# Optimization experiments

Measured on AMD Instinct MI355X. Metric: run time of the kernel, lower is better.

## Reference

```python
import jax, jax.numpy as jnp
import numpy as np
from jax import lax


def _prelu(x, a):
    return jnp.where(x >= 0, x, a * x)


def setup_inputs() -> dict:
    key = jax.random.key(0)
    ks = jax.random.split(key, 6)
    T, B, I, H = 2048, 64, 256, 256
    return {
        "sequences": jax.random.normal(ks[0], (T, B, I), dtype=jnp.float32),
        "W_f": jax.random.normal(ks[1], (I, H), dtype=jnp.float32) * (2.0 / (I + H)) ** 0.5,
        "U_f": jax.random.normal(ks[2], (H, H), dtype=jnp.float32) * (1.0 / H) ** 0.5,
        "b_f": jnp.ones((H,), dtype=jnp.float32),  # chrono-init bias ~ log(U(1,T_max))
        "W_h": jax.random.normal(ks[3], (I, H), dtype=jnp.float32) * (2.0 / (I + H)) ** 0.5,
        "U_h": jax.random.normal(ks[4], (H, H), dtype=jnp.float32) * (1.0 / H) ** 0.5,
        "b_h": jnp.zeros((H,), dtype=jnp.float32),
        "prelu_a": jnp.full((1,), 0.25, dtype=jnp.float32),
    }


def reference(sequences, W_f, U_f, b_f, W_h, U_h, b_h, prelu_a):
    # sequences: [T, B, I] time-major. Precompute input projections once
    # (hoists the big GEMMs out of the sequential recurrence).
    xf = jnp.einsum('tbi,ih->tbh', sequences, W_f) + b_f  # [T,B,H]
    xh = jnp.einsum('tbi,ih->tbh', sequences, W_h) + b_h  # [T,B,H]

    # First step: last_h is None -> no U terms, no f*last_h term.
    f0 = jax.nn.sigmoid(xf[0])
    h0 = _prelu((1.0 - f0) * jnp.tanh(xh[0]), prelu_a)  # [B,H]

    def step(h, xs):
        xf_t, xh_t = xs
        f = jax.nn.sigmoid(h @ U_f + xf_t)
        h_new = f * h + (1.0 - f) * jnp.tanh(h @ U_h + xh_t)
        h_new = _prelu(h_new, prelu_a)
        return h_new, h_new

    _, hs = lax.scan(step, h0, (xf[1:], xh[1:]))  # [T-1,B,H]
    all_h = jnp.concatenate([h0[None], hs], axis=0)  # [T,B,H]
    # torch.cat(hs) concatenates along dim 0 -> [T*B, H]
    return all_h.reshape(-1, all_h.shape[-1])
```

## Files before the change

kernel.cpp:

```cpp
#include <hip/hip_runtime.h>


#define T_STEPS 2048
#define BATCH   64
#define NCOL    512

typedef _Float16 half_t;
typedef half_t half2_t __attribute__((ext_vector_type(2)));
typedef half_t half4_t __attribute__((ext_vector_type(4)));

__device__ __forceinline__ float4 ld4(const float* p) { return *(const float4*)p; }
__device__ __forceinline__ void fma4(float4& acc, float s, const float4& v) {
  acc.x = fmaf(s, v.x, acc.x); acc.y = fmaf(s, v.y, acc.y);
  acc.z = fmaf(s, v.z, acc.z); acc.w = fmaf(s, v.w, acc.w);
}

__device__ __forceinline__ void store_xt(float* p, const float4& v) { *(float4*)p = v; }
__device__ __forceinline__ void store_xt(half_t* p, const float4& v) {
  half4_t h;
  h.x = (half_t)v.x; h.y = (half_t)v.y; h.z = (half_t)v.z; h.w = (half_t)v.w;
  *(half4_t*)p = h;
}
__device__ __forceinline__ float xload(const float* p) { return *p; }
__device__ __forceinline__ float xload(const half_t* p) { return (float)*p; }

#if __has_builtin(__builtin_amdgcn_fdot2)
__device__ __forceinline__ float fdot2(half2_t a, half2_t b, float c) {
  return __builtin_amdgcn_fdot2(a, b, c, false);
}
#else
__device__ __forceinline__ float fdot2(half2_t a, half2_t b, float c) {
  return c + (float)a.x * (float)b.x + (float)a.y * (float)b.y;
}
#endif

__device__ __forceinline__ half2_t bcast_h2(float f) {
  return __builtin_bit_cast(half2_t, f);
}

template <typename XT>
__global__ __launch_bounds__(256, 4)
void xproj_gemm(const float* __restrict__ seq,
                const float* __restrict__ Wf, const float* __restrict__ bf,
                const float* __restrict__ Wh, const float* __restrict__ bh,
                XT* __restrict__ xfh)
{
  __shared__ float As[32 * 132];
  __shared__ float Bs[32 * 132];
  const int tid = threadIdx.x;
  const int mt = blockIdx.x >> 2;
  const int nt = blockIdx.x & 3;
  const int m0 = mt * 128;
  const int n0 = nt * 128;
  const int tm = tid >> 4;
  const int tn = tid & 15;

  float4 acc[8][2];
  #pragma unroll
  for (int i = 0; i < 8; ++i) {
    acc[i][0] = make_float4(0.f, 0.f, 0.f, 0.f);
    acc[i][1] = make_float4(0.f, 0.f, 0.f, 0.f);
  }

  const float* bsrc  = (n0 < 256) ? Wf : Wh;
  const int    bcol0 = (n0 < 256) ? n0 : (n0 - 256);

  for (int kt = 0; kt < 8; ++kt) {
    const int k0 = kt * 32;
    #pragma unroll
    for (int p = 0; p < 4; ++p) {
      int idx = p * 256 + tid;
      int r   = idx >> 3;
      int c4  = idx & 7;
      float4 v = ld4(seq + (size_t)(m0 + r) * 256 + k0 + c4 * 4);
      As[(c4*4+0)*132 + r] = v.x;
      As[(c4*4+1)*132 + r] = v.y;
      As[(c4*4+2)*132 + r] = v.z;
      As[(c4*4+3)*132 + r] = v.w;
    }
    #pragma unroll
    for (int p = 0; p < 4; ++p) {
      int idx = p * 256 + tid;
      int kr  = idx >> 5;
      int c4  = idx & 31;
      float4 v = ld4(bsrc + (size_t)(k0 + kr) * 256 + bcol0 + c4 * 4);
      *(float4*)&Bs[kr*132 + c4*4] = v;
    }
    __syncthreads();
    #pragma unroll
    for (int k = 0; k < 32; ++k) {
      float4 a0 = ld4(&As[k*132 + tm*4]);
      float4 a1 = ld4(&As[k*132 + 64 + tm*4]);
      float4 b0 = ld4(&Bs[k*132 + tn*4]);
      float4 b1 = ld4(&Bs[k*132 + 64 + tn*4]);
      float ar[8] = {a0.x, a0.y, a0.z, a0.w, a1.x, a1.y, a1.z, a1.w};
      #pragma unroll
      for (int i = 0; i < 8; ++i) {
        fma4(acc[i][0], ar[i], b0);
        fma4(acc[i][1], ar[i], b1);
      }
    }
    __syncthreads();
  }

  const float* bias_src = (n0 < 256) ? bf : bh;
  float4 bias0 = ld4(bias_src + bcol0 + tn*4);
  float4 bias1 = ld4(bias_src + bcol0 + 64 + tn*4);
  #pragma unroll
  for (int i = 0; i < 8; ++i) {
    int m = m0 + ((i < 4) ? (tm*4 + i) : (64 + tm*4 + (i - 4)));
    float4 r0 = acc[i][0];
    r0.x += bias0.x; r0.y += bias0.y; r0.z += bias0.z; r0.w += bias0.w;
    float4 r1 = acc[i][1];
    r1.x += bias1.x; r1.y += bias1.y; r1.z += bias1.z; r1.w += bias1.w;
    store_xt(xfh + (size_t)m * NCOL + n0 + tn*4,      r0);
    store_xt(xfh + (size_t)m * NCOL + n0 + 64 + tn*4, r1);
  }
}

template <typename XT>
__global__ __launch_bounds__(512, 2)
void janet_rec(const float* __restrict__ Uf, const float* __restrict__ Uh,
               const XT* __restrict__ xfh, const float* __restrict__ pa,
               float* __restrict__ out)
{
  __shared__ __align__(16) half_t h_lds[256];
  __shared__ float g_lds[256];
  const int tid = threadIdx.x;
  const int b   = blockIdx.x;
  const int kg  = tid & 7;
  const int jg  = tid >> 3;
  const int j0  = jg * 8;

  const float* Usrc = (j0 < 256) ? (Uf + j0) : (Uh + (j0 - 256));
  half2_t u2[8][16];
  #pragma unroll
  for (int p = 0; p < 16; ++p) {
    const int k = kg * 32 + 2 * p;
    #pragma unroll
    for (int j = 0; j < 8; ++j) {
      half2_t w;
      w.x = (half_t)Usrc[(size_t)k * 256 + j];
      w.y = (half_t)Usrc[(size_t)(k + 1) * 256 + j];
      u2[j][p] = w;
    }
  }

  const float aprelu = pa[0];
  if (tid < 256) h_lds[tid] = (half_t)0.f;
  float h_old = 0.f;
  __syncthreads();

  float x = xload(xfh + (size_t)b * NCOL + tid);

  for (int t = 0; t < T_STEPS; ++t) {
    float x_next = 0.f;
    if (t + 1 < T_STEPS)
      x_next = xload(xfh + ((size_t)(t + 1) * BATCH + b) * NCOL + tid);

    const float4* hv4 = (const float4*)(h_lds + kg * 32);
    float4 ha = hv4[0], hb = hv4[1], hc = hv4[2], hd = hv4[3];
    half2_t hp[16];
    hp[0]  = bcast_h2(ha.x); hp[1]  = bcast_h2(ha.y);
    hp[2]  = bcast_h2(ha.z); hp[3]  = bcast_h2(ha.w);
    hp[4]  = bcast_h2(hb.x); hp[5]  = bcast_h2(hb.y);
    hp[6]  = bcast_h2(hb.z); hp[7]  = bcast_h2(hb.w);
    hp[8]  = bcast_h2(hc.x); hp[9]  = bcast_h2(hc.y);
    hp[10] = bcast_h2(hc.z); hp[11] = bcast_h2(hc.w);
    hp[12] = bcast_h2(hd.x); hp[13] = bcast_h2(hd.y);
    hp[14] = bcast_h2(hd.z); hp[15] = bcast_h2(hd.w);

    float acc[8];
    #pragma unroll
    for (int j = 0; j < 8; ++j) acc[j] = 0.f;
    #pragma unroll
    for (int p = 0; p < 16; ++p) {
      const half2_t hv = hp[p];
      #pragma unroll
      for (int j = 0; j < 8; ++j)
        acc[j] = fdot2(hv, u2[j][p], acc[j]);
    }

    float s00 = acc[0] + __shfl_xor(acc[0], 1);
    float s01 = acc[1] + __shfl_xor(acc[1], 1);
    float s02 = acc[2] + __shfl_xor(acc[2], 1);
    float s03 = acc[3] + __shfl_xor(acc[3], 1);
    float s04 = acc[4] + __shfl_xor(acc[4], 1);
    float s05 = acc[5] + __shfl_xor(acc[5], 1);
    float s06 = acc[6] + __shfl_xor(acc[6], 1);
    float s07 = acc[7] + __shfl_xor(acc[7], 1);
    const bool sb0 = (kg & 1);
    float r0 = sb0 ? s01 : s00;
    float r1 = sb0 ? s03 : s02;
    float r2 = sb0 ? s05 : s04;
    float r3 = sb0 ? s07 : s06;
    r0 += __shfl_xor(r0, 2);
    r1 += __shfl_xor(r1, 2);
    r2 += __shfl_xor(r2, 2);
    r3 += __shfl_xor(r3, 2);
    const bool sb1 = (kg & 2);
    float q0 = sb1 ? r1 : r0;
    float q1 = sb1 ? r3 : r2;
    q0 += __shfl_xor(q0, 4);
    q1 += __shfl_xor(q1, 4);
    const float s = (kg & 4) ? q1 : q0;

    const float pre = s + x;
    float f = 0.f;
    if (tid < 256) {
      f = __builtin_amdgcn_rcpf(1.f + __expf(-pre));
    } else {
      float e2 = __expf(2.f * pre);
      float g  = 1.f - 2.f * __builtin_amdgcn_rcpf(e2 + 1.f);
      g_lds[tid - 256] = g;
    }
    __syncthreads();
    if (tid < 256) {
      float g  = g_lds[tid];
      float hn = fmaf(f, h_old - g, g);
      hn = (hn >= 0.f) ? hn : aprelu * hn;
      h_old = hn;
      h_lds[tid] = (half_t)hn;
      out[((size_t)t * BATCH + b) * 256 + tid] = hn;
    }
    __syncthreads();
    x = x_next;
  }
}

extern "C" void kernel_launch(void* const* d_in, const int* in_sizes, int n_in,
                              void* d_out, int out_size, void* d_ws, size_t ws_size,
                              hipStream_t stream) {
  const float* seq = (const float*)d_in[0];
  const float* Wf  = (const float*)d_in[1];
  const float* Uf  = (const float*)d_in[2];
  const float* bf  = (const float*)d_in[3];
  const float* Wh  = (const float*)d_in[4];
  const float* Uh  = (const float*)d_in[5];
  const float* bh  = (const float*)d_in[6];
  const float* pa  = (const float*)d_in[7];
  float* out = (float*)d_out;

  const size_t rows = (size_t)T_STEPS * BATCH;
  const size_t need_f32 = rows * NCOL * sizeof(float);

  dim3 g1(4096), blk1(256);
  dim3 g2(BATCH), blk2(512);

  if (ws_size >= need_f32) {
    float* xfh = (float*)d_ws;
    hipLaunchKernelGGL(xproj_gemm<float>, g1, blk1, 0, stream, seq, Wf, bf, Wh, bh, xfh);
    hipLaunchKernelGGL(janet_rec<float>,  g2, blk2, 0, stream, Uf, Uh, xfh, pa, out);
  } else {
    half_t* xfh = (half_t*)d_ws;
    hipLaunchKernelGGL(xproj_gemm<half_t>, g1, blk1, 0, stream, seq, Wf, bf, Wh, bh, xfh);
    hipLaunchKernelGGL(janet_rec<half_t>,  g2, blk2, 0, stream, Uf, Uh, xfh, pa, out);
  }
}
```

Measured before the change: 2.533 ms.

## Use MFMA for the recurrent matmul with 16 batch rows per block

Replaces the per-batch fdot2 recurrence with MFMA 16x16x32 f16 instructions. Each block now handles 16 batch rows, and each wave computes a 32-column slice of both the f and h gates, so the gate math fuses with no cross-thread g exchange. Hidden state is double-buffered in swizzled LDS, which needs only one barrier per step. The grid shrinks from 64 blocks to 4, so far fewer CUs are used, and the per-step x loads are no longer prefetched.

```diff
diff --git a/kernel.cpp b/kernel.cpp
--- a/kernel.cpp
+++ b/kernel.cpp
@@ -4,10 +4,12 @@
 #define T_STEPS 2048
 #define BATCH   64
 #define NCOL    512
+#define MB      16
 
 typedef _Float16 half_t;
-typedef half_t half2_t __attribute__((ext_vector_type(2)));
+typedef half_t f16x8  __attribute__((ext_vector_type(8)));
 typedef half_t half4_t __attribute__((ext_vector_type(4)));
+typedef float  f32x4  __attribute__((ext_vector_type(4)));
 
 __device__ __forceinline__ float4 ld4(const float* p) { return *(const float4*)p; }
 __device__ __forceinline__ void fma4(float4& acc, float s, const float4& v) {
@@ -23,20 +25,6 @@
 }
 __device__ __forceinline__ float xload(const float* p) { return *p; }
 __device__ __forceinline__ float xload(const half_t* p) { return (float)*p; }
-
-#if __has_builtin(__builtin_amdgcn_fdot2)
-__device__ __forceinline__ float fdot2(half2_t a, half2_t b, float c) {
-  return __builtin_amdgcn_fdot2(a, b, c, false);
-}
-#else
-__device__ __forceinline__ float fdot2(half2_t a, half2_t b, float c) {
-  return c + (float)a.x * (float)b.x + (float)a.y * (float)b.y;
-}
-#endif
-
-__device__ __forceinline__ half2_t bcast_h2(float f) {
-  return __builtin_bit_cast(half2_t, f);
-}
 
 template <typename XT>
 __global__ __launch_bounds__(256, 4)
@@ -124,107 +112,113 @@
                const XT* __restrict__ xfh, const float* __restrict__ pa,
                float* __restrict__ out)
 {
-  __shared__ __align__(16) half_t h_lds[256];
-  __shared__ float g_lds[256];
-  const int tid = threadIdx.x;
-  const int b   = blockIdx.x;
-  const int kg  = tid & 7;
-  const int jg  = tid >> 3;
-  const int j0  = jg * 8;
-
-  const float* Usrc = (j0 < 256) ? (Uf + j0) : (Uh + (j0 - 256));
-  half2_t u2[8][16];
-  #pragma unroll
-  for (int p = 0; p < 16; ++p) {
-    const int k = kg * 32 + 2 * p;
-    #pragma unroll
-    for (int j = 0; j < 8; ++j) {
-      half2_t w;
-      w.x = (half_t)Usrc[(size_t)k * 256 + j];
-      w.y = (half_t)Usrc[(size_t)(k + 1) * 256 + j];
-      u2[j][p] = w;
+  __shared__ __align__(16) half_t hbuf[2][MB * 256];
+  const int tid  = threadIdx.x;
+  const int wave = tid >> 6;
+  const int lane = tid & 63;
+  const int l15  = lane & 15;
+  const int lk   = lane >> 4;
+  const int wcol = wave * 32;
+
+  f16x8 u[4][8];
+  #pragma unroll
+  for (int nt = 0; nt < 4; ++nt) {
+    const float* Us = (nt < 2) ? Uf : Uh;
+    const int col = wcol + (nt & 1) * 16 + l15;
+    #pragma unroll
+    for (int kt = 0; kt < 8; ++kt) {
+      const int k0 = kt * 32 + lk * 8;
+      f16x8 v;
+      #pragma unroll
+      for (int e = 0; e < 8; ++e) v[e] = (half_t)Us[(size_t)(k0 + e) * 256 + col];
+      u[nt][kt] = v;
     }
   }
 
   const float aprelu = pa[0];
-  if (tid < 256) h_lds[tid] = (half_t)0.f;
-  float h_old = 0.f;
+  const int b0 = lk * 4;
+
+  {
+    f16x8 z;
+    #pragma unroll
+    for (int e = 0; e < 8; ++e) z[e] = (half_t)0.f;
+    *(f16x8*)&hbuf[0][tid * 8] = z;
+  }
   __syncthreads();
 
-  float x = xload(xfh + (size_t)b * NCOL + tid);
+  float h_old[2][4];
+  #pragma unroll
+  for (int n = 0; n < 2; ++n)
+    #pragma unroll
+    for (int r = 0; r < 4; ++r) h_old[n][r] = 0.f;
+
+  const XT* xp[4];
+  float*    op[4];
+  #pragma unroll
+  for (int r = 0; r < 4; ++r) {
+    const int bg = blockIdx.x * MB + b0 + r;
+    xp[r] = xfh + (size_t)bg * NCOL + wcol + l15;
+    op[r] = out + (size_t)bg * 256  + wcol + l15;
+  }
+
+  const char* hb   = (const char*)hbuf;
+  const int   swzA = (l15 & 7) << 4;
+  const int   arow = l15 * 512 + lk * 16;
+  int pb = 0;
 
   for (int t = 0; t < T_STEPS; ++t) {
-    float x_next = 0.f;
-    if (t + 1 < T_STEPS)
-      x_next = xload(xfh + ((size_t)(t + 1) * BATCH + b) * NCOL + tid);
-
-    const float4* hv4 = (const float4*)(h_lds + kg * 32);
-    float4 ha = hv4[0], hb = hv4[1], hc = hv4[2], hd = hv4[3];
-    half2_t hp[16];
-    hp[0]  = bcast_h2(ha.x); hp[1]  = bcast_h2(ha.y);
-    hp[2]  = bcast_h2(ha.z); hp[3]  = bcast_h2(ha.w);
-    hp[4]  = bcast_h2(hb.x); hp[5]  = bcast_h2(hb.y);
-    hp[6]  = bcast_h2(hb.z); hp[7]  = bcast_h2(hb.w);
-    hp[8]  = bcast_h2(hc.x); hp[9]  = bcast_h2(hc.y);
-    hp[10] = bcast_h2(hc.z); hp[11] = bcast_h2(hc.w);
-    hp[12] = bcast_h2(hd.x); hp[13] = bcast_h2(hd.y);
-    hp[14] = bcast_h2(hd.z); hp[15] = bcast_h2(hd.w);
-
-    float acc[8];
-    #pragma unroll
-    for (int j = 0; j < 8; ++j) acc[j] = 0.f;
-    #pragma unroll
-    for (int p = 0; p < 16; ++p) {
-      const half2_t hv = hp[p];
-      #pragma unroll
-      for (int j = 0; j < 8; ++j)
-        acc[j] = fdot2(hv, u2[j][p], acc[j]);
-    }
-
-    float s00 = acc[0] + __shfl_xor(acc[0], 1);
-    float s01 = acc[1] + __shfl_xor(acc[1], 1);
-    float s02 = acc[2] + __shfl_xor(acc[2], 1);
-    float s03 = acc[3] + __shfl_xor(acc[3], 1);
-    float s04 = acc[4] + __shfl_xor(acc[4], 1);
-    float s05 = acc[5] + __shfl_xor(acc[5], 1);
-    float s06 = acc[6] + __shfl_xor(acc[6], 1);
-    float s07 = acc[7] + __shfl_xor(acc[7], 1);
-    const bool sb0 = (kg & 1);
-    float r0 = sb0 ? s01 : s00;
-    float r1 = sb0 ? s03 : s02;
-    float r2 = sb0 ? s05 : s04;
-    float r3 = sb0 ? s07 : s06;
-    r0 += __shfl_xor(r0, 2);
-    r1 += __shfl_xor(r1, 2);
-    r2 += __shfl_xor(r2, 2);
-    r3 += __shfl_xor(r3, 2);
-    const bool sb1 = (kg & 2);
-    float q0 = sb1 ? r1 : r0;
-    float q1 = sb1 ? r3 : r2;
-    q0 += __shfl_xor(q0, 4);
-    q1 += __shfl_xor(q1, 4);
-    const float s = (kg & 4) ? q1 : q0;
-
-    const float pre = s + x;
-    float f = 0.f;
-    if (tid < 256) {
-      f = __builtin_amdgcn_rcpf(1.f + __expf(-pre));
-    } else {
-      float e2 = __expf(2.f * pre);
-      float g  = 1.f - 2.f * __builtin_amdgcn_rcpf(e2 + 1.f);
-      g_lds[tid - 256] = g;
-    }
+    float xf[2][4], xh[2][4];
+    #pragma unroll
+    for (int r = 0; r < 4; ++r) {
+      xf[0][r] = xload(xp[r] + 0);
+      xf[1][r] = xload(xp[r] + 16);
+      xh[0][r] = xload(xp[r] + 256);
+      xh[1][r] = xload(xp[r] + 272);
+      xp[r] += (size_t)BATCH * NCOL;
+    }
+
+    f16x8 a[8];
+    #pragma unroll
+    for (int kt = 0; kt < 8; ++kt) {
+      const int off = pb + ((arow + kt * 64) ^ swzA);
+      a[kt] = *(const f16x8*)(hb + off);
+    }
+
+    f32x4 acc[4];
+    #pragma unroll
+    for (int nt = 0; nt < 4; ++nt) {
+      acc[nt][0] = 0.f; acc[nt][1] = 0.f; acc[nt][2] = 0.f; acc[nt][3] = 0.f;
+    }
+    #pragma unroll
+    for (int kt = 0; kt < 8; ++kt) {
+      #pragma unroll
+      for (int nt = 0; nt < 4; ++nt)
+        acc[nt] = __builtin_amdgcn_mfma_f32_16x16x32_f16(a[kt], u[nt][kt], acc[nt], 0, 0, 0);
+    }
+
+    const int wb = pb ^ (int)sizeof(hbuf[0]);
+    #pragma unroll
+    for (int n = 0; n < 2; ++n) {
+      #pragma unroll
+      for (int r = 0; r < 4; ++r) {
+        const float pf = acc[n][r]     + xf[n][r];
+        const float pg = acc[n + 2][r] + xh[n][r];
+        const float f  = __builtin_amdgcn_rcpf(1.f + __expf(-pf));
+        const float e2 = __expf(2.f * pg);
+        const float g  = 1.f - 2.f * __builtin_amdgcn_rcpf(e2 + 1.f);
+        float hn = fmaf(f, h_old[n][r] - g, g);
+        hn = (hn >= 0.f) ? hn : aprelu * hn;
+        h_old[n][r] = hn;
+        op[r][n * 16] = hn;
+        const int brow = b0 + r;
+        const int woff = wb + ((brow * 512 + (wcol + n * 16 + l15) * 2) ^ ((brow & 7) << 4));
+        *(half_t*)((char*)hbuf + woff) = (half_t)hn;
+      }
+    }
+    #pragma unroll
+    for (int r = 0; r < 4; ++r) op[r] += (size_t)BATCH * 256;
     __syncthreads();
-    if (tid < 256) {
-      float g  = g_lds[tid];
-      float hn = fmaf(f, h_old - g, g);
-      hn = (hn >= 0.f) ? hn : aprelu * hn;
-      h_old = hn;
-      h_lds[tid] = (half_t)hn;
-      out[((size_t)t * BATCH + b) * 256 + tid] = hn;
-    }
-    __syncthreads();
-    x = x_next;
+    pb = wb;
   }
 }
 
@@ -245,7 +239,7 @@
   const size_t need_f32 = rows * NCOL * sizeof(float);
 
   dim3 g1(4096), blk1(256);
-  dim3 g2(BATCH), blk2(512);
+  dim3 g2(BATCH / MB), blk2(512);
 
   if (ws_size >= need_f32) {
     float* xfh = (float*)d_ws;
```

Measured after the change: 4.064 ms. 60.5% more time.

## Pair f/h gate columns per thread group to drop one barrier per step

Applied to the files above, without the earlier changes.

Each thread group now computes 4 f-columns and the matching 4 h-columns, so the sigmoid and tanh results are combined with an intra-wave shuffle instead of through an LDS buffer. This removes one of the two block barriers per timestep. The h vector is stored in a swizzled LDS layout so that reads avoid bank conflicts. The loop is unrolled by two with double-buffered x prefetch, the barrier is issued manually with an explicit lgkmcnt wait, and PReLU becomes branchless. Every thread now does the gate arithmetic, and the raw barrier plus swizzle indexing carry correctness risk.

```diff
diff --git a/kernel.cpp b/kernel.cpp
--- a/kernel.cpp
+++ b/kernel.cpp
@@ -119,113 +119,129 @@
 }
 
 template <typename XT>
-__global__ __launch_bounds__(512, 2)
+__global__ __launch_bounds__(512)
+__attribute__((amdgpu_waves_per_eu(2, 2)))
 void janet_rec(const float* __restrict__ Uf, const float* __restrict__ Uh,
                const XT* __restrict__ xfh, const float* __restrict__ pa,
                float* __restrict__ out)
 {
   __shared__ __align__(16) half_t h_lds[256];
-  __shared__ float g_lds[256];
   const int tid = threadIdx.x;
   const int b   = blockIdx.x;
   const int kg  = tid & 7;
   const int jg  = tid >> 3;
-  const int j0  = jg * 8;
-
-  const float* Usrc = (j0 < 256) ? (Uf + j0) : (Uh + (j0 - 256));
+  const int j0  = jg * 4;
+
   half2_t u2[8][16];
   #pragma unroll
-  for (int p = 0; p < 16; ++p) {
-    const int k = kg * 32 + 2 * p;
-    #pragma unroll
-    for (int j = 0; j < 8; ++j) {
+  for (int i = 0; i < 8; ++i) {
+    const float* Us = (i < 4) ? (Uf + j0 + i) : (Uh + j0 + i - 4);
+    #pragma unroll
+    for (int p = 0; p < 16; ++p) {
+      const int k = kg * 32 + 2 * p;
       half2_t w;
-      w.x = (half_t)Usrc[(size_t)k * 256 + j];
-      w.y = (half_t)Usrc[(size_t)(k + 1) * 256 + j];
-      u2[j][p] = w;
+      w.x = (half_t)Us[(size_t)k * 256];
+      w.y = (half_t)Us[(size_t)(k + 1) * 256];
+      u2[i][p] = w;
     }
   }
 
   const float aprelu = pa[0];
+
+  const int ocol = j0 + (kg & 3);
+  const int xcol = (kg < 4) ? ocol : (256 + ocol);
+  const XT* xp = xfh + (size_t)b * NCOL + xcol;
+  float*   op  = out + (size_t)b * 256 + ocol;
+
+  const char* hrd = (const char*)h_lds + kg * 16;
+  int wbyte;
+  {
+    const int c = ocol >> 3;
+    const int P = ((c & 3) << 3) | (c >> 2);
+    wbyte = (P * 8 + (ocol & 7)) * 2;
+  }
+
   if (tid < 256) h_lds[tid] = (half_t)0.f;
   float h_old = 0.f;
-  __syncthreads();
-
-  float x = xload(xfh + (size_t)b * NCOL + tid);
-
-  for (int t = 0; t < T_STEPS; ++t) {
-    float x_next = 0.f;
-    if (t + 1 < T_STEPS)
-      x_next = xload(xfh + ((size_t)(t + 1) * BATCH + b) * NCOL + tid);
-
-    const float4* hv4 = (const float4*)(h_lds + kg * 32);
-    float4 ha = hv4[0], hb = hv4[1], hc = hv4[2], hd = hv4[3];
-    half2_t hp[16];
-    hp[0]  = bcast_h2(ha.x); hp[1]  = bcast_h2(ha.y);
-    hp[2]  = bcast_h2(ha.z); hp[3]  = bcast_h2(ha.w);
-    hp[4]  = bcast_h2(hb.x); hp[5]  = bcast_h2(hb.y);
-    hp[6]  = bcast_h2(hb.z); hp[7]  = bcast_h2(hb.w);
-    hp[8]  = bcast_h2(hc.x); hp[9]  = bcast_h2(hc.y);
-    hp[10] = bcast_h2(hc.z); hp[11] = bcast_h2(hc.w);
-    hp[12] = bcast_h2(hd.x); hp[13] = bcast_h2(hd.y);
-    hp[14] = bcast_h2(hd.z); hp[15] = bcast_h2(hd.w);
-
-    float acc[8];
-    #pragma unroll
-    for (int j = 0; j < 8; ++j) acc[j] = 0.f;
-    #pragma unroll
-    for (int p = 0; p < 16; ++p) {
-      const half2_t hv = hp[p];
-      #pragma unroll
-      for (int j = 0; j < 8; ++j)
-        acc[j] = fdot2(hv, u2[j][p], acc[j]);
-    }
-
-    float s00 = acc[0] + __shfl_xor(acc[0], 1);
-    float s01 = acc[1] + __shfl_xor(acc[1], 1);
-    float s02 = acc[2] + __shfl_xor(acc[2], 1);
-    float s03 = acc[3] + __shfl_xor(acc[3], 1);
-    float s04 = acc[4] + __shfl_xor(acc[4], 1);
-    float s05 = acc[5] + __shfl_xor(acc[5], 1);
-    float s06 = acc[6] + __shfl_xor(acc[6], 1);
-    float s07 = acc[7] + __shfl_xor(acc[7], 1);
-    const bool sb0 = (kg & 1);
-    float r0 = sb0 ? s01 : s00;
-    float r1 = sb0 ? s03 : s02;
-    float r2 = sb0 ? s05 : s04;
-    float r3 = sb0 ? s07 : s06;
-    r0 += __shfl_xor(r0, 2);
-    r1 += __shfl_xor(r1, 2);
-    r2 += __shfl_xor(r2, 2);
-    r3 += __shfl_xor(r3, 2);
-    const bool sb1 = (kg & 2);
-    float q0 = sb1 ? r1 : r0;
-    float q1 = sb1 ? r3 : r2;
-    q0 += __shfl_xor(q0, 4);
-    q1 += __shfl_xor(q1, 4);
-    const float s = (kg & 4) ? q1 : q0;
-
-    const float pre = s + x;
-    float f = 0.f;
-    if (tid < 256) {
-      f = __builtin_amdgcn_rcpf(1.f + __expf(-pre));
-    } else {
-      float e2 = __expf(2.f * pre);
-      float g  = 1.f - 2.f * __builtin_amdgcn_rcpf(e2 + 1.f);
-      g_lds[tid - 256] = g;
-    }
-    __syncthreads();
-    if (tid < 256) {
-      float g  = g_lds[tid];
-      float hn = fmaf(f, h_old - g, g);
-      hn = (hn >= 0.f) ? hn : aprelu * hn;
-      h_old = hn;
-      h_lds[tid] = (half_t)hn;
-      out[((size_t)t * BATCH + b) * 256 + tid] = hn;
-    }
-    __syncthreads();
-    x = x_next;
-  }
+
+  float xA = xload(xp); xp += (size_t)BATCH * NCOL;
+  float xB = xload(xp); xp += (size_t)BATCH * NCOL;
+
+  asm volatile("s_waitcnt lgkmcnt(0)" ::: "memory");
+  __builtin_amdgcn_s_barrier();
+  asm volatile("" ::: "memory");
+
+#define JSTEP(t, xb)                                                            \
+  {                                                                             \
+    const float4 q0 = *(const float4*)(hrd + 0);                                \
+    const float4 q1 = *(const float4*)(hrd + 128);                              \
+    const float4 q2 = *(const float4*)(hrd + 256);                              \
+    const float4 q3 = *(const float4*)(hrd + 384);                              \
+    half2_t hp[16];                                                             \
+    hp[0]  = bcast_h2(q0.x); hp[1]  = bcast_h2(q0.y);                           \
+    hp[2]  = bcast_h2(q0.z); hp[3]  = bcast_h2(q0.w);                           \
+    hp[4]  = bcast_h2(q1.x); hp[5]  = bcast_h2(q1.y);                           \
+    hp[6]  = bcast_h2(q1.z); hp[7]  = bcast_h2(q1.w);                           \
+    hp[8]  = bcast_h2(q2.x); hp[9]  = bcast_h2(q2.y);                           \
+    hp[10] = bcast_h2(q2.z); hp[11] = bcast_h2(q2.w);                           \
+    hp[12] = bcast_h2(q3.x); hp[13] = bcast_h2(q3.y);                           \
+    hp[14] = bcast_h2(q3.z); hp[15] = bcast_h2(q3.w);                           \
+    float acc[8];                                                               \
+    _Pragma("unroll")                                                           \
+    for (int i = 0; i < 8; ++i) acc[i] = 0.f;                                   \
+    _Pragma("unroll")                                                           \
+    for (int p = 0; p < 16; ++p) {                                              \
+      const half2_t hv = hp[p];                                                 \
+      _Pragma("unroll")                                                         \
+      for (int i = 0; i < 8; ++i) acc[i] = fdot2(hv, u2[i][p], acc[i]);         \
+    }                                                                           \
+    float s00 = acc[0] + __shfl_xor(acc[0], 1);                                 \
+    float s01 = acc[1] + __shfl_xor(acc[1], 1);                                 \
+    float s02 = acc[2] + __shfl_xor(acc[2], 1);                                 \
+    float s03 = acc[3] + __shfl_xor(acc[3], 1);                                 \
+    float s04 = acc[4] + __shfl_xor(acc[4], 1);                                 \
+    float s05 = acc[5] + __shfl_xor(acc[5], 1);                                 \
+    float s06 = acc[6] + __shfl_xor(acc[6], 1);                                 \
+    float s07 = acc[7] + __shfl_xor(acc[7], 1);                                 \
+    const bool sb0 = (kg & 1);                                                  \
+    float r0 = sb0 ? s01 : s00;                                                 \
+    float r1 = sb0 ? s03 : s02;                                                 \
+    float r2 = sb0 ? s05 : s04;                                                 \
+    float r3 = sb0 ? s07 : s06;                                                 \
+    r0 += __shfl_xor(r0, 2);                                                    \
+    r1 += __shfl_xor(r1, 2);                                                    \
+    r2 += __shfl_xor(r2, 2);                                                    \
+    r3 += __shfl_xor(r3, 2);                                                    \
+    const bool sb1 = (kg & 2);                                                  \
+    float t0 = sb1 ? r1 : r0;                                                   \
+    float t1 = sb1 ? r3 : r2;                                                   \
+    t0 += __shfl_xor(t0, 4);                                                    \
+    t1 += __shfl_xor(t1, 4);                                                    \
+    const float dsum = (kg & 4) ? t1 : t0;                                      \
+    const float pre = dsum + xb;                                                \
+    const float e   = __expf((kg < 4) ? -pre : 2.f * pre);                      \
+    const float rr  = __builtin_amdgcn_rcpf(1.f + e);                           \
+    const float val = (kg < 4) ? rr : fmaf(-2.f, rr, 1.f);                      \
+    const float oth = __shfl_xor(val, 4);                                       \
+    const float fg_f = (kg < 4) ? val : oth;                                    \
+    const float fg_g = (kg < 4) ? oth : val;                                    \
+    float hn = fmaf(fg_f, h_old - fg_g, fg_g);                                  \
+    hn = fmaf(aprelu, fminf(hn, 0.f), fmaxf(hn, 0.f));               \
+    h_old = hn;                                                                 \
+    if (kg < 4) *(half_t*)((char*)h_lds + wbyte) = (half_t)hn;                  \
+    else        *op = hn;                                                       \
+    op += (size_t)BATCH * 256;                                                  \
+    if ((t) + 2 < T_STEPS) { xb = xload(xp); xp += (size_t)BATCH * NCOL; }      \
+    asm volatile("s_waitcnt lgkmcnt(0)" ::: "memory");                          \
+    __builtin_amdgcn_s_barrier();                                               \
+    asm volatile("" ::: "memory");                                              \
+  }
+
+  for (int t = 0; t < T_STEPS; t += 2) {
+    JSTEP(t,     xA);
+    JSTEP(t + 1, xB);
+  }
+#undef JSTEP
 }
 
 extern "C" void kernel_launch(void* const* d_in, const int* in_sizes, int n_in,
```

New measurement: 2.467 ms. -2.6%, faster.
